# Kernel optimization log

Hardware: AMD Instinct MI355X
Metric: run time of the kernel (lower is better)

## Reference

```python
import jax, jax.numpy as jnp
import numpy as np

NUM_HEADS = 32
HEAD_DIM = 128
ROPE_THETA = 10000.0


def _rope_tables(seq_len, head_dim, theta):
    inv_freq = 1.0 / (theta ** (jnp.arange(0, head_dim, 2, dtype=jnp.float32) / head_dim))
    pos = jnp.arange(seq_len, dtype=jnp.float32)
    freqs = pos[:, None] * inv_freq[None, :]            # [S, hd/2]
    emb = jnp.concatenate([freqs, freqs], axis=-1)      # [S, hd]
    return jnp.cos(emb), jnp.sin(emb)


def _rotate_half(x):
    x1, x2 = jnp.split(x, 2, axis=-1)
    return jnp.concatenate([-x2, x1], axis=-1)


def _apply_rope(x, cos, sin):
    # x: [B, S, H, D]; cos/sin: [S, D] -> unsqueeze_dim=2 broadcasting
    c = cos[None, :, None, :]
    s = sin[None, :, None, :]
    return x * c + _rotate_half(x) * s


def setup_inputs() -> dict:
    key = jax.random.key(0)
    ks = jax.random.split(key, 6)
    hidden = 4096
    B, S = 2, 4096  # global sequence = world_size * local_seq (4 * 1024)
    hidden_states = jax.random.normal(ks[0], (B, S, hidden), dtype=jnp.float32)
    # original uses torch.rand (uniform); scaled by 0.02 for numerical sanity
    q_proj = jax.random.uniform(ks[1], (hidden, hidden), dtype=jnp.float32) * 0.02
    k_proj = jax.random.uniform(ks[2], (hidden, hidden), dtype=jnp.float32) * 0.02
    v_proj = jax.random.uniform(ks[3], (hidden, hidden), dtype=jnp.float32) * 0.02
    o_proj = jax.random.uniform(ks[4], (hidden, hidden), dtype=jnp.float32) * 0.02
    return {"hidden_states": hidden_states, "q_proj": q_proj, "k_proj": k_proj,
            "v_proj": v_proj, "o_proj": o_proj, "world_size": 4}


def _ring_attention(hidden_states, q_proj, k_proj, v_proj, o_proj, world_size):
    B, S, H = hidden_states.shape
    s_local = S // world_size
    nh, hd = NUM_HEADS, HEAD_DIM
    scale = 1.0 / np.sqrt(hd).astype(np.float32)

    # rank 0 holds the first sequence shard as its local hidden states
    hs_local = hidden_states[:, :s_local]
    q = (hs_local @ q_proj.T).reshape(B, s_local, nh, hd)
    k = (hidden_states @ k_proj.T).reshape(B, S, nh, hd)
    v = (hidden_states @ v_proj.T).reshape(B, S, nh, hd)

    cos, sin = _rope_tables(S, hd, ROPE_THETA)
    q = _apply_rope(q, cos[:s_local], sin[:s_local])   # rank0 positions 0..s_local-1
    k = _apply_rope(k, cos, sin)                       # global positions per shard

    # split into per-rank KV blocks; rank 0 receives blocks W-1, W-2, ..., 0
    k_blocks = k.reshape(B, world_size, s_local, nh, hd).transpose(1, 0, 2, 3, 4)[::-1]
    v_blocks = v.reshape(B, world_size, s_local, nh, hd).transpose(1, 0, 2, 3, 4)[::-1]

    def step(carry, kv):
        attn, max_lse, denom, lse_full = carry
        k_blk, v_blk = kv
        # memory_efficient_attention_partial: non-causal partial attention + lse
        s = jnp.einsum('bqhd,bkhd->bhqk', q, k_blk) * scale
        m = jnp.max(s, axis=-1)                          # [B,H,q]
        p = jnp.exp(s - m[..., None])
        l = jnp.sum(p, axis=-1)
        lse = (m + jnp.log(l)).transpose(0, 2, 1)        # [B,q,H]
        out = jnp.einsum('bhqk,bkhd->bqhd', p / l[..., None], v_blk)
        # online-softmax merge across ring steps
        new_max = jnp.maximum(max_lse, lse)
        old_adj = jnp.exp(max_lse - new_max)[..., None]
        new_adj = jnp.exp(lse - new_max)[..., None]
        denom = old_adj * denom + new_adj
        attn = old_adj * attn + new_adj * out
        lse_full = new_max + jnp.log(jnp.exp(lse_full - new_max) + jnp.exp(lse - new_max))
        return (attn, new_max, denom, lse_full), None

    init = (jnp.zeros((B, s_local, nh, hd), jnp.float32),
            jnp.full((B, s_local, nh), -jnp.inf, jnp.float32),
            jnp.zeros((B, s_local, nh, 1), jnp.float32),
            jnp.full((B, s_local, nh), -jnp.inf, jnp.float32))
    (attn, _, denom, _), _ = jax.lax.scan(step, init, (k_blocks, v_blocks))

    attn = attn / denom
    attn = attn.astype(jnp.float16).astype(jnp.float32)  # .half() in source
    attn = attn.reshape(B, s_local, nh * hd)
    return attn @ o_proj.T


def reference(hidden_states, q_proj, k_proj, v_proj, o_proj, world_size):
    return _ring_attention(hidden_states, q_proj, k_proj, v_proj, o_proj, world_size)
```

## Files before the change

kernel.cpp:

```cpp
#include <hip/hip_runtime.h>


using bf16x8 = __attribute__((ext_vector_type(8))) short;
using f32x4  = __attribute__((ext_vector_type(4))) float;

__device__ inline unsigned short f32_to_bf16_bits(float f) {
  unsigned int u = __float_as_uint(f);
  u += 0x7FFFu + ((u >> 16) & 1u);
  return (unsigned short)(u >> 16);
}
__device__ inline float bf16_bits_to_f32(unsigned short h) {
  return __uint_as_float(((unsigned int)h) << 16);
}

__device__ __forceinline__ void load_lds16(const unsigned short* g, unsigned short* l) {
  __builtin_amdgcn_global_load_lds(
      (const __attribute__((address_space(1))) void*)g,
      (__attribute__((address_space(3))) void*)l, 16, 0, 0);
}

__global__ void cast_f32_bf16_batched(const float* __restrict__ hs,
                                      const float* __restrict__ w0,
                                      const float* __restrict__ w1,
                                      const float* __restrict__ w2,
                                      const float* __restrict__ w3,
                                      unsigned short* __restrict__ out) {
  const long hs4 = 2L * 4096 * 4096 / 4;
  const long w4  = 4096L * 4096 / 4;
  long i = (long)blockIdx.x * blockDim.x + threadIdx.x;
  long stride = (long)gridDim.x * blockDim.x;
  const long total = hs4 + 4 * w4;
  for (; i < total; i += stride) {
    const float* src;
    long j = i;
    if (j < hs4) { src = hs; }
    else {
      j -= hs4;
      long wi = j / w4;
      j -= wi * w4;
      src = (wi == 0) ? w0 : (wi == 1) ? w1 : (wi == 2) ? w2 : w3;
    }
    float4 v = reinterpret_cast<const float4*>(src)[j];
    ushort4 o;
    o.x = f32_to_bf16_bits(v.x);
    o.y = f32_to_bf16_bits(v.y);
    o.z = f32_to_bf16_bits(v.z);
    o.w = f32_to_bf16_bits(v.w);
    reinterpret_cast<ushort4*>(out)[i] = o;
  }
}

__global__ void rope_tables(float* __restrict__ cos_t, float* __restrict__ sin_t) {
  int idx = blockIdx.x * 256 + threadIdx.x;
  if (idx >= 4096 * 64) return;
  int p = idx >> 6, i = idx & 63;
  float inv = __expf(-(float)i * (9.210340371976184f / 64.0f));
  float f = (float)p * inv;
  cos_t[idx] = cosf(f);
  sin_t[idx] = sinf(f);
}

__global__ void rope_apply_v(unsigned short* __restrict__ buf,
                             const float4* __restrict__ cos4,
                             const float4* __restrict__ sin4,
                             long nchunks, int pos_mask, float gain) {
  long idx = (long)blockIdx.x * 256 + threadIdx.x;
  if (idx >= nchunks) return;
  long tok = idx >> 8;
  int rem = (int)(idx & 255);
  int head = rem >> 3, c = rem & 7;
  int pos = (int)(tok & (long)pos_mask);
  float4 ct0 = cos4[pos * 16 + c * 2];
  float4 ct1 = cos4[pos * 16 + c * 2 + 1];
  float4 st0 = sin4[pos * 16 + c * 2];
  float4 st1 = sin4[pos * 16 + c * 2 + 1];
  float cs[8] = {ct0.x, ct0.y, ct0.z, ct0.w, ct1.x, ct1.y, ct1.z, ct1.w};
  float sn[8] = {st0.x, st0.y, st0.z, st0.w, st1.x, st1.y, st1.z, st1.w};
  long base = tok * 4096 + head * 128 + c * 8;
  bf16x8 x1 = *reinterpret_cast<const bf16x8*>(buf + base);
  bf16x8 x2 = *reinterpret_cast<const bf16x8*>(buf + base + 64);
  bf16x8 o1, o2;
#pragma unroll
  for (int j = 0; j < 8; j++) {
    float a = bf16_bits_to_f32((unsigned short)x1[j]);
    float b = bf16_bits_to_f32((unsigned short)x2[j]);
    o1[j] = (short)f32_to_bf16_bits((a * cs[j] - b * sn[j]) * gain);
    o2[j] = (short)f32_to_bf16_bits((b * cs[j] + a * sn[j]) * gain);
  }
  *reinterpret_cast<bf16x8*>(buf + base) = o1;
  *reinterpret_cast<bf16x8*>(buf + base + 64) = o2;
}

__device__ inline void storeC(float* p, float v) { *p = v; }
__device__ inline void storeC(unsigned short* p, float v) { *p = f32_to_bf16_bits(v); }

template <typename OUT_T>
__global__ __launch_bounds__(256) void gemm_bt(const unsigned short* __restrict__ A,
                                               const unsigned short* __restrict__ B,
                                               OUT_T* __restrict__ C,
                                               long Astride_z, long Cstride_z, int N) {
  __shared__ unsigned short As[128 * 32];
  __shared__ unsigned short Bs[128 * 32];
  const int tid = threadIdx.x;
  const int bn = blockIdx.x, bm = blockIdx.y, bz = blockIdx.z;
  const unsigned short* Ab = A + (long)bz * Astride_z + (long)bm * 128 * 4096;
  const unsigned short* Bb = B + (long)bn * 128 * 4096;
  OUT_T* Cb = C + (long)bz * Cstride_z + (long)bm * 128 * N + (long)bn * 128;

  const int lane = tid & 63;
  const int w = tid >> 6;
  const int wr = (w >> 1) * 64, wc = (w & 1) * 64;
  const int fr = lane & 15, fg = lane >> 4;

  f32x4 acc[4][4] = {};

  const int c0 = tid, c1 = tid + 256;
  const int rA0 = c0 >> 2, kc0 = c0 & 3;
  const int rA1 = c1 >> 2, kc1 = c1 & 3;

  for (int k0 = 0; k0 < 4096; k0 += 32) {
    load_lds16(Ab + (long)rA0 * 4096 + k0 + kc0 * 8, As + c0 * 8);
    load_lds16(Ab + (long)rA1 * 4096 + k0 + kc1 * 8, As + c1 * 8);
    load_lds16(Bb + (long)rA0 * 4096 + k0 + kc0 * 8, Bs + c0 * 8);
    load_lds16(Bb + (long)rA1 * 4096 + k0 + kc1 * 8, Bs + c1 * 8);
    __syncthreads();
    bf16x8 af[4], bfv[4];
#pragma unroll
    for (int m = 0; m < 4; m++)
      af[m] = *reinterpret_cast<const bf16x8*>(As + (wr + m * 16 + fr) * 32 + fg * 8);
#pragma unroll
    for (int n = 0; n < 4; n++)
      bfv[n] = *reinterpret_cast<const bf16x8*>(Bs + (wc + n * 16 + fr) * 32 + fg * 8);
#pragma unroll
    for (int m = 0; m < 4; m++)
#pragma unroll
      for (int n = 0; n < 4; n++)
        acc[m][n] = __builtin_amdgcn_mfma_f32_16x16x32_bf16(af[m], bfv[n], acc[m][n], 0, 0, 0);
    __syncthreads();
  }
#pragma unroll
  for (int m = 0; m < 4; m++)
#pragma unroll
    for (int n = 0; n < 4; n++)
#pragma unroll
      for (int r = 0; r < 4; r++) {
        int row = wr + m * 16 + fg * 4 + r;
        int col = wc + n * 16 + fr;
        storeC(Cb + (long)row * N + col, acc[m][n][r]);
      }
}

#define STG2(Gb, Lb, h, kc)                                                    \
  load_lds16((Gb) + (long)((h) * 128 + srow) * 4096 + sslot * 8 + (kc),        \
             (Lb) + tid * 8);                                                  \
  load_lds16((Gb) + (long)((h) * 128 + 64 + srow) * 4096 + sslot * 8 + (kc),   \
             (Lb) + 4096 + tid * 8);

#define MFMAQ(MH, NH)                                                          \
  _Pragma("unroll") for (int mi = 0; mi < 4; ++mi)                             \
    _Pragma("unroll") for (int ni = 0; ni < 2; ++ni)                           \
      _Pragma("unroll") for (int kk = 0; kk < 2; ++kk)                         \
        acc[(MH) * 4 + mi][(NH) * 2 + ni] =                                    \
            __builtin_amdgcn_mfma_f32_16x16x32_bf16(                           \
                a[mi][kk], b[(NH) * 2 + ni][kk],                               \
                acc[(MH) * 4 + mi][(NH) * 2 + ni], 0, 0, 0);

#define TILE(P, KC, MODE)                                                      \
  {                                                                            \
    const unsigned short* Ar = lds + wm * 16384 + (P) * 8192;                  \
    const unsigned short* Br =                                                 \
        lds + 32768 + (wn >> 1) * 16384 + (P) * 8192 + (wn & 1) * 4096;        \
    _Pragma("unroll") for (int mf = 0; mf < 4; ++mf) {                         \
      a[mf][0] = *reinterpret_cast<const bf16x8*>(Ar + mf * 1024 + ao0);       \
      a[mf][1] = *reinterpret_cast<const bf16x8*>(Ar + mf * 1024 + ao1);       \
    }                                                                          \
    _Pragma("unroll") for (int nf = 0; nf < 2; ++nf) {                         \
      b[nf][0] = *reinterpret_cast<const bf16x8*>(Br + nf * 1024 + ao0);       \
      b[nf][1] = *reinterpret_cast<const bf16x8*>(Br + nf * 1024 + ao1);       \
    }                                                                          \
    __builtin_amdgcn_s_setprio(1);                                             \
    MFMAQ(0, 0);                                                               \
    __builtin_amdgcn_s_setprio(0);                                             \
    _Pragma("unroll") for (int nf = 2; nf < 4; ++nf) {                         \
      b[nf][0] = *reinterpret_cast<const bf16x8*>(Br + nf * 1024 + ao0);       \
      b[nf][1] = *reinterpret_cast<const bf16x8*>(Br + nf * 1024 + ao1);       \
    }                                                                          \
    __builtin_amdgcn_s_setprio(1);                                             \
    MFMAQ(0, 1);                                                               \
    __builtin_amdgcn_s_setprio(0);                                             \
    asm volatile("s_waitcnt lgkmcnt(0)" ::: "memory");                         \
    asm volatile("s_barrier" ::: "memory");            \
    if ((MODE) == 0) {                                                         \
      STG2(Bg, lds + 32768 + (P) * 8192, 0, KC);                               \
      STG2(Bg, lds + 49152 + (P) * 8192, 1, KC);                               \
    }                                                                          \
    _Pragma("unroll") for (int mf = 0; mf < 4; ++mf) {                         \
      a[mf][0] = *reinterpret_cast<const bf16x8*>(Ar + (4 + mf) * 1024 + ao0); \
      a[mf][1] = *reinterpret_cast<const bf16x8*>(Ar + (4 + mf) * 1024 + ao1); \
    }                                                                          \
    __builtin_amdgcn_s_setprio(1);                                             \
    MFMAQ(1, 0);                                                               \
    __builtin_amdgcn_s_setprio(0);                                             \
    asm volatile("s_waitcnt lgkmcnt(0)" ::: "memory");                         \
    asm volatile("s_barrier" ::: "memory");            \
    if ((MODE) == 0) {                                                         \
      STG2(Ag, lds + (P) * 8192, 0, KC);                                       \
      STG2(Ag, lds + 16384 + (P) * 8192, 1, KC);                               \
    }                                                                          \
    __builtin_amdgcn_s_setprio(1);                                             \
    MFMAQ(1, 1);                                                               \
    __builtin_amdgcn_s_setprio(0);                                             \
    if ((MODE) == 0) asm volatile("s_waitcnt vmcnt(8)" ::: "memory");          \
    if ((MODE) == 1) asm volatile("s_waitcnt vmcnt(0)" ::: "memory");          \
    asm volatile("s_barrier" ::: "memory");       \
  }

template <typename OUT_T>
__global__ __launch_bounds__(512, 2) void gemm256(const unsigned short* __restrict__ A,
                                                  const unsigned short* __restrict__ B,
                                                  OUT_T* __restrict__ C,
                                                  long Astride_z, long Cstride_z, int N) {
  __shared__ unsigned short lds[65536];
  const int tid = threadIdx.x;
  const int bn = blockIdx.x, bm = blockIdx.y, bz = blockIdx.z;
  const unsigned short* Ag = A + (long)bz * Astride_z + (long)bm * 256 * 4096;
  const unsigned short* Bg = B + (long)bn * 256 * 4096;

  const int w = tid >> 6, lane = tid & 63;
  const int wm = w >> 2, wn = w & 3;
  const int fr = lane & 15, fg = lane >> 4;
  const int ao0 = fr * 64 + ((fg ^ (fr & 7)) * 8);
  const int ao1 = fr * 64 + (((4 + fg) ^ (fr & 7)) * 8);
  const int srow = tid >> 3;
  const int sslot = (tid & 7) ^ (srow & 7);

  f32x4 acc[8][4] = {};
  bf16x8 a[4][2], b[4][2];

  STG2(Ag, lds + 0, 0, 0);     STG2(Ag, lds + 16384, 1, 0);
  STG2(Bg, lds + 32768, 0, 0); STG2(Bg, lds + 49152, 1, 0);
  STG2(Ag, lds + 8192, 0, 64);  STG2(Ag, lds + 24576, 1, 64);
  STG2(Bg, lds + 40960, 0, 64); STG2(Bg, lds + 57344, 1, 64);
  asm volatile("s_waitcnt vmcnt(8)" ::: "memory");
  asm volatile("s_barrier" ::: "memory");

  for (int ti = 0; ti < 31; ++ti) {
    TILE(0, (2 * ti + 2) * 64, 0);
    TILE(1, (2 * ti + 3) * 64, 0);
  }
  TILE(0, 0, 1);
  TILE(1, 0, 2);

  OUT_T* Cb = C + (long)bz * Cstride_z + ((long)bm * 256) * N + bn * 256;
#pragma unroll
  for (int mf = 0; mf < 8; ++mf)
#pragma unroll
    for (int nf = 0; nf < 4; ++nf)
#pragma unroll
      for (int rr = 0; rr < 4; ++rr) {
        int row = wm * 128 + mf * 16 + fg * 4 + rr;
        int col = wn * 64 + nf * 16 + fr;
        storeC(Cb + (long)row * N + col, acc[mf][nf][rr]);
      }
}

#define AT_STAGE(P, kv)                                                        \
  _Pragma("unroll") for (int i = 0; i < 4; i++) {                              \
    int c = tid + 256 * i;                                                     \
    int key = c >> 4, s0 = c & 15;                                             \
    int Lg = s0 ^ (key & 15);                                                  \
    load_lds16(kbase + (long)((kv) + key) * 4096 + Lg * 8, &Ks[P][c * 8]);     \
  }                                                                            \
  _Pragma("unroll") for (int i = 0; i < 4; i++) {                              \
    int c = tid + 256 * i;                                                     \
    int f0 = c >> 3, s0 = c & 7;                                               \
    int Lg = s0 ^ (f0 & 7);                                                    \
    load_lds16(vbase + (long)f0 * 8192 + (kv) + Lg * 8, &Vl[P][c * 8]);        \
  }

__global__ __launch_bounds__(256) void attn_fwd(const unsigned short* __restrict__ qb,
                                                const unsigned short* __restrict__ kb,
                                                const unsigned short* __restrict__ vT,
                                                unsigned short* __restrict__ ob) {
  __shared__ unsigned short Ks[2][64 * 128];
  __shared__ unsigned short Vl[2][128 * 64];
  __shared__ unsigned short Ps[4][16 * 72];

  const int qt = blockIdx.x, h = blockIdx.y, b = blockIdx.z;
  const int tid = threadIdx.x, w = tid >> 6, lane = tid & 63;
  const int fr = lane & 15, fg = lane >> 4;

  const unsigned short* kbase = kb + (long)b * 4096 * 4096 + h * 128;
  const unsigned short* vbase = vT + (long)h * 128 * 8192 + (long)b * 4096;

  bf16x8 qf[4];
  {
    const unsigned short* qptr =
        qb + ((long)b * 1024 + qt * 64 + w * 16 + fr) * 4096 + h * 128 + fg * 8;
#pragma unroll
    for (int c = 0; c < 4; c++) qf[c] = *reinterpret_cast<const bf16x8*>(qptr + c * 32);
  }

  f32x4 outa[8] = {};
  float m_run[4], l_run[4];
#pragma unroll
  for (int r = 0; r < 4; r++) { m_run[r] = -1e30f; l_run[r] = 0.0f; }

  AT_STAGE(0, 0);
  asm volatile("s_waitcnt vmcnt(0)" ::: "memory");
  asm volatile("s_barrier" ::: "memory");

  for (int t = 0; t < 64; ++t) {
    const int cur = t & 1;
    if (t < 63) { AT_STAGE(cur ^ 1, (t + 1) * 64); }

    f32x4 sacc[4];
    __builtin_amdgcn_s_setprio(1);
#pragma unroll
    for (int ks = 0; ks < 4; ks++) {
      f32x4 aq = {0.f, 0.f, 0.f, 0.f};
#pragma unroll
      for (int cc = 0; cc < 4; cc++) {
        bf16x8 kf = *reinterpret_cast<const bf16x8*>(
            &Ks[cur][(ks * 16 + fr) * 128 + (((cc * 4 + fg) ^ fr) & 15) * 8]);
        aq = __builtin_amdgcn_mfma_f32_16x16x32_bf16(qf[cc], kf, aq, 0, 0, 0);
      }
      sacc[ks] = aq;
    }
    __builtin_amdgcn_s_setprio(0);

    float mxl[4];
    int need = 0;
#pragma unroll
    for (int r = 0; r < 4; r++) {
      mxl[r] = fmaxf(fmaxf(sacc[0][r], sacc[1][r]), fmaxf(sacc[2][r], sacc[3][r]));
      need |= (mxl[r] > m_run[r] + 11.5f) ? 1 : 0;
    }
    if (__any(need)) {
#pragma unroll
      for (int r = 0; r < 4; r++) {
        float mx = mxl[r];
        mx = fmaxf(mx, __shfl_xor(mx, 1));
        mx = fmaxf(mx, __shfl_xor(mx, 2));
        mx = fmaxf(mx, __shfl_xor(mx, 4));
        mx = fmaxf(mx, __shfl_xor(mx, 8));
        float mnew = fmaxf(m_run[r], mx);
        float ef = exp2f(m_run[r] - mnew);
        l_run[r] *= ef;
        m_run[r] = mnew;
#pragma unroll
        for (int ds = 0; ds < 8; ds++) outa[ds][r] *= ef;
      }
    }
#pragma unroll
    for (int r = 0; r < 4; r++) {
      float sum = 0.f;
#pragma unroll
      for (int ks = 0; ks < 4; ks++) {
        float pv = exp2f(sacc[ks][r] - m_run[r]);
        Ps[w][(fg * 4 + r) * 72 + ks * 16 + fr] = f32_to_bf16_bits(pv);
        sum += pv;
      }
      l_run[r] += sum;
    }

    __builtin_amdgcn_s_setprio(1);
#pragma unroll
    for (int c2 = 0; c2 < 2; c2++) {
      bf16x8 pf = *reinterpret_cast<const bf16x8*>(&Ps[w][fr * 72 + c2 * 32 + fg * 8]);
#pragma unroll
      for (int ds = 0; ds < 8; ds++) {
        int feat = ds * 16 + fr;
        int pch = ((c2 * 4 + fg) ^ (feat & 7)) & 7;
        bf16x8 vf = *reinterpret_cast<const bf16x8*>(&Vl[cur][feat * 64 + pch * 8]);
        outa[ds] = __builtin_amdgcn_mfma_f32_16x16x32_bf16(pf, vf, outa[ds], 0, 0, 0);
      }
    }
    __builtin_amdgcn_s_setprio(0);

    if (t < 63) {
      asm volatile("s_waitcnt vmcnt(0) lgkmcnt(0)" ::: "memory");
      asm volatile("s_barrier" ::: "memory");
    }
  }

#pragma unroll
  for (int r = 0; r < 4; r++) {
    float l = l_run[r];
    l += __shfl_xor(l, 1);
    l += __shfl_xor(l, 2);
    l += __shfl_xor(l, 4);
    l += __shfl_xor(l, 8);
    float inv = 1.0f / l;
    unsigned short* op =
        ob + ((long)b * 1024 + qt * 64 + w * 16 + fg * 4 + r) * 4096 + h * 128;
#pragma unroll
    for (int ds = 0; ds < 8; ds++) op[ds * 16 + fr] = f32_to_bf16_bits(outa[ds][r] * inv);
  }
}

extern "C" void kernel_launch(void* const* d_in, const int* in_sizes, int n_in,
                              void* d_out, int out_size, void* d_ws, size_t ws_size,
                              hipStream_t stream) {
  const float* hs = (const float*)d_in[0];
  const float* wq = (const float*)d_in[1];
  const float* wk = (const float*)d_in[2];
  const float* wv = (const float*)d_in[3];
  const float* wo = (const float*)d_in[4];
  float* out = (float*)d_out;

  const long hsN = 2L * 4096 * 4096;
  const long wN  = 4096L * 4096;

  unsigned short* hs_b = (unsigned short*)d_ws;
  unsigned short* wq_b = hs_b + hsN;
  unsigned short* wk_b = wq_b + wN;
  unsigned short* wv_b = wk_b + wN;
  unsigned short* wo_b = wv_b + wN;
  unsigned short* q_b  = wo_b + wN;
  unsigned short* k_b  = q_b + 2048L * 4096;
  unsigned short* vT_b = k_b + 8192L * 4096;
  unsigned short* at_b = vT_b + 8192L * 4096;
  float* cos_t = (float*)(at_b + 2048L * 4096);
  float* sin_t = cos_t + 4096 * 64;

  cast_f32_bf16_batched<<<dim3(8192), dim3(256), 0, stream>>>(
      hs, wq, wk, wv, wo, hs_b);

  rope_tables<<<dim3(1024), dim3(256), 0, stream>>>(cos_t, sin_t);

  gemm_bt<unsigned short><<<dim3(32, 8, 2), dim3(256), 0, stream>>>(
      hs_b, wq_b, q_b, 4096L * 4096, 1024L * 4096, 4096);
  gemm256<unsigned short><<<dim3(16, 16, 2), dim3(512), 0, stream>>>(
      hs_b, wk_b, k_b, 4096L * 4096, 4096L * 4096, 4096);
  gemm256<unsigned short><<<dim3(32, 16, 1), dim3(512), 0, stream>>>(
      wv_b, hs_b, vT_b, 0L, 0L, 8192);

  const float qgain = 0.08838834764831845f * 1.4426950408889634f;
  rope_apply_v<<<dim3(2048), dim3(256), 0, stream>>>(
      q_b, (const float4*)cos_t, (const float4*)sin_t, 2048L * 256, 1023, qgain);
  rope_apply_v<<<dim3(8192), dim3(256), 0, stream>>>(
      k_b, (const float4*)cos_t, (const float4*)sin_t, 8192L * 256, 4095, 1.0f);

  attn_fwd<<<dim3(16, 32, 2), dim3(256), 0, stream>>>(q_b, k_b, vT_b, at_b);

  gemm_bt<float><<<dim3(32, 16, 1), dim3(256), 0, stream>>>(
      at_b, wo_b, out, 0L, 0L, 4096);
}
```

Measured before the change: 1.022 ms.

## Switch attention kernel to 32x32x16 MFMA with 128-query tiles and 32-key blocks

Rewrites the attention inner loop to use 32x32x16 bf16 MFMA instead of 16x16x32. Each wave now owns 32 query rows, so a block covers 128 queries and the grid halves. Each K/V block in LDS shrinks to 32 keys, with new XOR swizzles for K, V and P. This is meant to halve K/V global and LDS traffic per query and use the denser MFMA shape. In exchange it raises register pressure (16 softmax rows per lane, 64 accumulators), runs twice as many loop iterations with barriers, and launches fewer blocks (512).

```diff
diff --git a/kernel.cpp b/kernel.cpp
--- a/kernel.cpp
+++ b/kernel.cpp
@@ -3,6 +3,7 @@
 
 using bf16x8 = __attribute__((ext_vector_type(8))) short;
 using f32x4  = __attribute__((ext_vector_type(4))) float;
+using f32x16 = __attribute__((ext_vector_type(16))) float;
 
 __device__ inline unsigned short f32_to_bf16_bits(float f) {
   unsigned int u = __float_as_uint(f);
@@ -265,16 +266,16 @@
 }
 
 #define AT_STAGE(P, kv)                                                        \
-  _Pragma("unroll") for (int i = 0; i < 4; i++) {                              \
+  _Pragma("unroll") for (int i = 0; i < 2; i++) {                              \
     int c = tid + 256 * i;                                                     \
     int key = c >> 4, s0 = c & 15;                                             \
     int Lg = s0 ^ (key & 15);                                                  \
     load_lds16(kbase + (long)((kv) + key) * 4096 + Lg * 8, &Ks[P][c * 8]);     \
   }                                                                            \
-  _Pragma("unroll") for (int i = 0; i < 4; i++) {                              \
+  _Pragma("unroll") for (int i = 0; i < 2; i++) {                              \
     int c = tid + 256 * i;                                                     \
-    int f0 = c >> 3, s0 = c & 7;                                               \
-    int Lg = s0 ^ (f0 & 7);                                                    \
+    int f0 = c >> 2, s0 = c & 3;                                               \
+    int Lg = s0 ^ (f0 & 3);                                                    \
     load_lds16(vbase + (long)f0 * 8192 + (kv) + Lg * 8, &Vl[P][c * 8]);        \
   }
 
@@ -282,120 +283,114 @@
                                                 const unsigned short* __restrict__ kb,
                                                 const unsigned short* __restrict__ vT,
                                                 unsigned short* __restrict__ ob) {
-  __shared__ unsigned short Ks[2][64 * 128];
-  __shared__ unsigned short Vl[2][128 * 64];
-  __shared__ unsigned short Ps[4][16 * 72];
+  __shared__ unsigned short Ks[2][32 * 128];
+  __shared__ unsigned short Vl[2][128 * 32];
+  __shared__ unsigned short Ps[4][32 * 40];
 
   const int qt = blockIdx.x, h = blockIdx.y, b = blockIdx.z;
   const int tid = threadIdx.x, w = tid >> 6, lane = tid & 63;
-  const int fr = lane & 15, fg = lane >> 4;
+  const int lq = lane & 31;
+  const int kg = lane >> 5;
 
   const unsigned short* kbase = kb + (long)b * 4096 * 4096 + h * 128;
   const unsigned short* vbase = vT + (long)h * 128 * 8192 + (long)b * 4096;
 
-  bf16x8 qf[4];
+  bf16x8 qf[8];
   {
     const unsigned short* qptr =
-        qb + ((long)b * 1024 + qt * 64 + w * 16 + fr) * 4096 + h * 128 + fg * 8;
-#pragma unroll
-    for (int c = 0; c < 4; c++) qf[c] = *reinterpret_cast<const bf16x8*>(qptr + c * 32);
-  }
-
-  f32x4 outa[8] = {};
-  float m_run[4], l_run[4];
-#pragma unroll
-  for (int r = 0; r < 4; r++) { m_run[r] = -1e30f; l_run[r] = 0.0f; }
+        qb + ((long)b * 1024 + qt * 128 + w * 32 + lq) * 4096 + h * 128 + kg * 8;
+#pragma unroll
+    for (int t = 0; t < 8; t++) qf[t] = *reinterpret_cast<const bf16x8*>(qptr + 16 * t);
+  }
+
+  f32x16 acc[4] = {};
+  float m_run[16], l_run[16];
+#pragma unroll
+  for (int r = 0; r < 16; r++) { m_run[r] = -1e30f; l_run[r] = 0.0f; }
 
   AT_STAGE(0, 0);
   asm volatile("s_waitcnt vmcnt(0)" ::: "memory");
   asm volatile("s_barrier" ::: "memory");
 
-  for (int t = 0; t < 64; ++t) {
+  for (int t = 0; t < 128; ++t) {
     const int cur = t & 1;
-    if (t < 63) { AT_STAGE(cur ^ 1, (t + 1) * 64); }
-
-    f32x4 sacc[4];
+    if (t < 127) { AT_STAGE(cur ^ 1, (t + 1) * 32); }
+
+    f32x16 sacc = {};
     __builtin_amdgcn_s_setprio(1);
 #pragma unroll
-    for (int ks = 0; ks < 4; ks++) {
-      f32x4 aq = {0.f, 0.f, 0.f, 0.f};
-#pragma unroll
-      for (int cc = 0; cc < 4; cc++) {
-        bf16x8 kf = *reinterpret_cast<const bf16x8*>(
-            &Ks[cur][(ks * 16 + fr) * 128 + (((cc * 4 + fg) ^ fr) & 15) * 8]);
-        aq = __builtin_amdgcn_mfma_f32_16x16x32_bf16(qf[cc], kf, aq, 0, 0, 0);
-      }
-      sacc[ks] = aq;
+    for (int ks = 0; ks < 8; ks++) {
+      bf16x8 kf = *reinterpret_cast<const bf16x8*>(
+          &Ks[cur][lq * 128 + (((2 * ks + kg) ^ (lq & 15)) & 15) * 8]);
+      sacc = __builtin_amdgcn_mfma_f32_32x32x16_bf16(qf[ks], kf, sacc, 0, 0, 0);
     }
     __builtin_amdgcn_s_setprio(0);
 
-    float mxl[4];
     int need = 0;
 #pragma unroll
-    for (int r = 0; r < 4; r++) {
-      mxl[r] = fmaxf(fmaxf(sacc[0][r], sacc[1][r]), fmaxf(sacc[2][r], sacc[3][r]));
-      need |= (mxl[r] > m_run[r] + 11.5f) ? 1 : 0;
-    }
+    for (int r = 0; r < 16; r++) need |= (sacc[r] > m_run[r] + 11.5f) ? 1 : 0;
     if (__any(need)) {
 #pragma unroll
-      for (int r = 0; r < 4; r++) {
-        float mx = mxl[r];
+      for (int r = 0; r < 16; r++) {
+        float mx = sacc[r];
         mx = fmaxf(mx, __shfl_xor(mx, 1));
         mx = fmaxf(mx, __shfl_xor(mx, 2));
         mx = fmaxf(mx, __shfl_xor(mx, 4));
         mx = fmaxf(mx, __shfl_xor(mx, 8));
+        mx = fmaxf(mx, __shfl_xor(mx, 16));
         float mnew = fmaxf(m_run[r], mx);
         float ef = exp2f(m_run[r] - mnew);
         l_run[r] *= ef;
         m_run[r] = mnew;
 #pragma unroll
-        for (int ds = 0; ds < 8; ds++) outa[ds][r] *= ef;
+        for (int d = 0; d < 4; d++) acc[d][r] *= ef;
       }
     }
 #pragma unroll
-    for (int r = 0; r < 4; r++) {
-      float sum = 0.f;
-#pragma unroll
-      for (int ks = 0; ks < 4; ks++) {
-        float pv = exp2f(sacc[ks][r] - m_run[r]);
-        Ps[w][(fg * 4 + r) * 72 + ks * 16 + fr] = f32_to_bf16_bits(pv);
-        sum += pv;
-      }
-      l_run[r] += sum;
-    }
-
+    for (int r = 0; r < 16; r++) {
+      float pv = exp2f(sacc[r] - m_run[r]);
+      int row = (r & 3) + 8 * (r >> 2) + 4 * kg;
+      Ps[w][row * 40 + (((lq >> 3) ^ (r >> 2)) << 3) + (lq & 7)] = f32_to_bf16_bits(pv);
+      l_run[r] += pv;
+    }
+
+    bf16x8 pa0 = *reinterpret_cast<const bf16x8*>(
+        &Ps[w][lq * 40 + ((kg ^ ((lq >> 3) & 3)) << 3)]);
+    bf16x8 pa1 = *reinterpret_cast<const bf16x8*>(
+        &Ps[w][lq * 40 + (((kg + 2) ^ ((lq >> 3) & 3)) << 3)]);
     __builtin_amdgcn_s_setprio(1);
 #pragma unroll
-    for (int c2 = 0; c2 < 2; c2++) {
-      bf16x8 pf = *reinterpret_cast<const bf16x8*>(&Ps[w][fr * 72 + c2 * 32 + fg * 8]);
-#pragma unroll
-      for (int ds = 0; ds < 8; ds++) {
-        int feat = ds * 16 + fr;
-        int pch = ((c2 * 4 + fg) ^ (feat & 7)) & 7;
-        bf16x8 vf = *reinterpret_cast<const bf16x8*>(&Vl[cur][feat * 64 + pch * 8]);
-        outa[ds] = __builtin_amdgcn_mfma_f32_16x16x32_bf16(pf, vf, outa[ds], 0, 0, 0);
-      }
+    for (int dsub = 0; dsub < 4; dsub++) {
+      bf16x8 v0 = *reinterpret_cast<const bf16x8*>(
+          &Vl[cur][(dsub * 32 + lq) * 32 + ((kg ^ (lq & 3)) << 3)]);
+      bf16x8 v1 = *reinterpret_cast<const bf16x8*>(
+          &Vl[cur][(dsub * 32 + lq) * 32 + (((kg + 2) ^ (lq & 3)) << 3)]);
+      acc[dsub] = __builtin_amdgcn_mfma_f32_32x32x16_bf16(pa0, v0, acc[dsub], 0, 0, 0);
+      acc[dsub] = __builtin_amdgcn_mfma_f32_32x32x16_bf16(pa1, v1, acc[dsub], 0, 0, 0);
     }
     __builtin_amdgcn_s_setprio(0);
 
-    if (t < 63) {
+    if (t < 127) {
       asm volatile("s_waitcnt vmcnt(0) lgkmcnt(0)" ::: "memory");
       asm volatile("s_barrier" ::: "memory");
     }
   }
 
 #pragma unroll
-  for (int r = 0; r < 4; r++) {
+  for (int r = 0; r < 16; r++) {
     float l = l_run[r];
     l += __shfl_xor(l, 1);
     l += __shfl_xor(l, 2);
     l += __shfl_xor(l, 4);
     l += __shfl_xor(l, 8);
+    l += __shfl_xor(l, 16);
     float inv = 1.0f / l;
+    int row = (r & 3) + 8 * (r >> 2) + 4 * kg;
     unsigned short* op =
-        ob + ((long)b * 1024 + qt * 64 + w * 16 + fg * 4 + r) * 4096 + h * 128;
-#pragma unroll
-    for (int ds = 0; ds < 8; ds++) op[ds * 16 + fr] = f32_to_bf16_bits(outa[ds][r] * inv);
+        ob + ((long)b * 1024 + qt * 128 + w * 32 + row) * 4096 + h * 128 + lq;
+#pragma unroll
+    for (int dsub = 0; dsub < 4; dsub++)
+      op[dsub * 32] = f32_to_bf16_bits(acc[dsub][r] * inv);
   }
 }
 
@@ -442,7 +437,7 @@
   rope_apply_v<<<dim3(8192), dim3(256), 0, stream>>>(
       k_b, (const float4*)cos_t, (const float4*)sin_t, 8192L * 256, 4095, 1.0f);
 
-  attn_fwd<<<dim3(16, 32, 2), dim3(256), 0, stream>>>(q_b, k_b, vT_b, at_b);
+  attn_fwd<<<dim3(8, 32, 2), dim3(256), 0, stream>>>(q_b, k_b, vT_b, at_b);
 
   gemm_bt<float><<<dim3(32, 16, 1), dim3(256), 0, stream>>>(
       at_b, wo_b, out, 0L, 0L, 4096);
```

Measured after the change: 1.220 ms. 19.4% more time.
